# Kernel tuning notes

Measured on AMD Instinct MI355X. Metric: run time of the kernel, lower is better.

## Reference

```python
import jax, jax.numpy as jnp
import numpy as np

N_NODES = 50000
NEG_SLOPE = 0.2


def gat_conv(x, W, att_src, att_dst, b, src, dst, n):
    # x: [N, F_in], W: [F_in, H*C], att_*: [H, C], b: [H*C]
    H, C = att_src.shape
    h = (x @ W).reshape(n, H, C)                       # [N, H, C]
    a_s = (h * att_src).sum(-1)                        # [N, H]
    a_d = (h * att_dst).sum(-1)                        # [N, H]
    e = jax.nn.leaky_relu(a_s[src] + a_d[dst], NEG_SLOPE)  # [E, H]
    # segment softmax over destination node (every node has a self-loop)
    m = jax.ops.segment_max(e, dst, num_segments=n)    # [N, H]
    ex = jnp.exp(e - m[dst])
    denom = jax.ops.segment_sum(ex, dst, num_segments=n)
    alpha = ex / denom[dst]                            # [E, H]
    out = jax.ops.segment_sum(alpha[:, :, None] * h[src], dst, num_segments=n)
    return out.reshape(n, H * C) + b


def setup_inputs() -> dict:
    key = jax.random.key(0)
    ks = jax.random.split(key, 10)
    n, e = N_NODES, 1600000
    x = jax.random.normal(ks[0], (n, 128), dtype=jnp.float32)
    edge_index = jax.random.randint(ks[1], (2, e), 0, n, dtype=jnp.int64)
    s = 0.1
    return {
        "x": x,
        "edge_index": edge_index,
        "W1": jax.random.normal(ks[2], (128, 128), dtype=jnp.float32) * s,
        "att_src1": jax.random.normal(ks[3], (4, 32), dtype=jnp.float32) * s,
        "att_dst1": jax.random.normal(ks[4], (4, 32), dtype=jnp.float32) * s,
        "b1": jnp.zeros((128,), dtype=jnp.float32),
        "W2": jax.random.normal(ks[5], (128, 128), dtype=jnp.float32) * s,
        "att_src2": jax.random.normal(ks[6], (4, 32), dtype=jnp.float32) * s,
        "att_dst2": jax.random.normal(ks[7], (4, 32), dtype=jnp.float32) * s,
        "b2": jnp.zeros((128,), dtype=jnp.float32),
    }


def reference(x, edge_index, W1, att_src1, att_dst1, b1, W2, att_src2, att_dst2, b2):
    n = x.shape[0]
    loops = jnp.arange(n, dtype=edge_index.dtype)
    src = jnp.concatenate([edge_index[0], loops])  # add self-loops (PyG default)
    dst = jnp.concatenate([edge_index[1], loops])
    h = gat_conv(x, W1, att_src1, att_dst1, b1, src, dst, n)
    h = jax.nn.relu(h)
    h = gat_conv(h, W2, att_src2, att_dst2, b2, src, dst, n)
    return (h, h)
```

## Files before the change

kernel.cpp:

```cpp
#include <hip/hip_runtime.h>
#include <hip/hip_bf16.h>


#define FDIM 128
#define NHEAD 4
#define NB 512

typedef __attribute__((ext_vector_type(16))) float f32x16;
typedef __attribute__((ext_vector_type(8)))  short s16x8;

__device__ inline unsigned short f2bf(float f) {
    union { float f; unsigned u; } v; v.f = f;
    unsigned r = v.u + 0x7fff + ((v.u >> 16) & 1);
    return (unsigned short)(r >> 16);
}
__device__ inline float2 bf2f(unsigned v) {
    union { unsigned u; float f; } a, b;
    a.u = v << 16;
    b.u = v & 0xffff0000u;
    return make_float2(a.f, b.f);
}

__global__ __launch_bounds__(256) void prep_w(const float* __restrict__ W,
                                              short* __restrict__ Bhi,
                                              short* __restrict__ Blo) {
    const int t = threadIdx.x;
    for (int i = 0; i < 64; i++) {
        int e = i * 256 + t;
        int k = e >> 7, n = e & 127;
        float f = W[e];
        unsigned u = __float_as_uint(f);
        unsigned short hi = (unsigned short)(u >> 16);
        float rem = f - __uint_as_float(u & 0xffff0000u);
        unsigned short lo = (unsigned short)(__float_as_uint(rem) >> 16);
        int idx = n * 128 + ((((k >> 3) ^ (n & 15))) << 3) + (k & 7);
        Bhi[idx] = (short)hi;
        Blo[idx] = (short)lo;
    }
}

__global__ __launch_bounds__(256) void gemm_mfma(const float* __restrict__ A,
                                                 const short* __restrict__ Bghi,
                                                 const short* __restrict__ Bglo,
                                                 unsigned short* __restrict__ H,
                                                 const float* __restrict__ att_s,
                                                 const float* __restrict__ att_d,
                                                 float* __restrict__ a_s,
                                                 float* __restrict__ a_d, int M) {
    __shared__ short Bsm[2][16384];
    __shared__ float attsm[256];
    const int t = threadIdx.x;
    const int bm = blockIdx.x * 64;

    if (t < 128) attsm[t] = att_s[t];
    else         attsm[t] = att_d[t - 128];

    {
        const uint4* ghi = (const uint4*)Bghi;
        const uint4* glo = (const uint4*)Bglo;
        uint4* shi = (uint4*)&Bsm[0][0];
        uint4* slo = (uint4*)&Bsm[1][0];
        #pragma unroll
        for (int i = 0; i < 8; i++) {
            shi[t + i * 256] = ghi[t + i * 256];
            slo[t + i * 256] = glo[t + i * 256];
        }
    }

    const int lane = t & 63;
    const int w = t >> 6;
    const int wr = w >> 1, wc = w & 1;
    const int m  = lane & 31, h2 = lane >> 5;
    const int grow = bm + wr * 32 + m;

    s16x8 ahi[8], alo[8];
    {
        const bool ok = grow < M;
        const float* ap = A + (size_t)grow * 128 + 8 * h2;
        #pragma unroll
        for (int c = 0; c < 8; c++) {
            float ff[8];
            if (ok) {
                float4 f0 = *(const float4*)(ap + c * 16);
                float4 f1 = *(const float4*)(ap + c * 16 + 4);
                ff[0]=f0.x; ff[1]=f0.y; ff[2]=f0.z; ff[3]=f0.w;
                ff[4]=f1.x; ff[5]=f1.y; ff[6]=f1.z; ff[7]=f1.w;
            } else {
                #pragma unroll
                for (int j = 0; j < 8; j++) ff[j] = 0.f;
            }
            #pragma unroll
            for (int j = 0; j < 8; j++) {
                unsigned u = __float_as_uint(ff[j]);
                float rem = ff[j] - __uint_as_float(u & 0xffff0000u);
                ahi[c][j] = (short)(u >> 16);
                alo[c][j] = (short)(__float_as_uint(rem) >> 16);
            }
        }
    }
    __syncthreads();

    f32x16 acc[2];
    #pragma unroll
    for (int i = 0; i < 16; i++) { acc[0][i] = 0.f; acc[1][i] = 0.f; }

    #pragma unroll
    for (int ni = 0; ni < 2; ni++) {
        const int n = ni * 64 + wc * 32 + m;
        const int nbase = n * 128;
        #pragma unroll
        for (int c = 0; c < 8; c++) {
            int chunk8 = 2 * c + h2;
            int koff = ((chunk8 ^ (n & 15)) << 3);
            s16x8 bhi = *(const s16x8*)&Bsm[0][nbase + koff];
            s16x8 blo = *(const s16x8*)&Bsm[1][nbase + koff];
            acc[ni] = __builtin_amdgcn_mfma_f32_32x32x16_bf16(ahi[c], bhi, acc[ni], 0, 0, 0);
            acc[ni] = __builtin_amdgcn_mfma_f32_32x32x16_bf16(alo[c], bhi, acc[ni], 0, 0, 0);
            acc[ni] = __builtin_amdgcn_mfma_f32_32x32x16_bf16(ahi[c], blo, acc[ni], 0, 0, 0);
        }
    }

    __syncthreads();
    unsigned short* htile = (unsigned short*)&Bsm[0][0];
    #pragma unroll
    for (int ni = 0; ni < 2; ni++) {
        const int colg = ni * 64 + wc * 32 + m;
        #pragma unroll
        for (int r = 0; r < 16; r++) {
            int row = wr * 32 + (r & 3) + 8 * (r >> 2) + 4 * h2;
            htile[row * 128 + colg] = (short)f2bf(acc[ni][r]);
        }
    }
    __syncthreads();

    {
        const int r = t >> 2, q = t & 3;
        const int growr = bm + r;
        if (growr < M) {
            uint4 v0 = *(uint4*)&htile[r * 128 + q * 32];
            uint4 v1 = *(uint4*)&htile[r * 128 + q * 32 + 8];
            uint4 v2 = *(uint4*)&htile[r * 128 + q * 32 + 16];
            uint4 v3 = *(uint4*)&htile[r * 128 + q * 32 + 24];
            uint4* hg = (uint4*)(H + (size_t)growr * 128);
            hg[q * 4 + 0] = v0; hg[q * 4 + 1] = v1;
            hg[q * 4 + 2] = v2; hg[q * 4 + 3] = v3;
            unsigned uu[16] = {v0.x, v0.y, v0.z, v0.w, v1.x, v1.y, v1.z, v1.w,
                               v2.x, v2.y, v2.z, v2.w, v3.x, v3.y, v3.z, v3.w};
            float ps = 0.f, pd = 0.f;
            #pragma unroll
            for (int i = 0; i < 16; i++) {
                float2 f = bf2f(uu[i]);
                ps += f.x * attsm[q * 32 + 2 * i]       + f.y * attsm[q * 32 + 2 * i + 1];
                pd += f.x * attsm[128 + q * 32 + 2 * i] + f.y * attsm[128 + q * 32 + 2 * i + 1];
            }
            a_s[growr * NHEAD + q] = ps;
            a_d[growr * NHEAD + q] = pd;
        }
    }
}

__global__ __launch_bounds__(256) void bucket_hist(const int* __restrict__ dst, int E,
                                                   unsigned long long magic,
                                                   int* __restrict__ bcnt) {
    __shared__ int sh[NB];
    const int t = threadIdx.x;
    for (int i = t; i < NB; i += 256) sh[i] = 0;
    __syncthreads();
    for (int i = blockIdx.x * blockDim.x + t; i < E; i += gridDim.x * blockDim.x) {
        int b = (int)(((unsigned long long)(unsigned)dst[i] * magic) >> 40);
        atomicAdd(&sh[b], 1);
    }
    __syncthreads();
    for (int i = t; i < NB; i += 256)
        if (sh[i]) atomicAdd(&bcnt[i], sh[i]);
}

__global__ __launch_bounds__(256) void bucket_scan(const int* __restrict__ bcnt,
                                                   int* __restrict__ bbase,
                                                   int* __restrict__ bcursor,
                                                   int* __restrict__ row_ptr,
                                                   int N, int E) {
    __shared__ int wsum[4];
    const int t = threadIdx.x, lane = t & 63, wid = t >> 6;
    int v0 = bcnt[2 * t], v1 = bcnt[2 * t + 1];
    int s = v0 + v1, incl = s;
    #pragma unroll
    for (int o = 1; o < 64; o <<= 1) {
        int u = __shfl_up(incl, o, 64);
        if (lane >= o) incl += u;
    }
    if (lane == 63) wsum[wid] = incl;
    __syncthreads();
    if (t == 0) {
        int a = 0;
        #pragma unroll
        for (int i = 0; i < 4; i++) { int x = wsum[i]; wsum[i] = a; a += x; }
    }
    __syncthreads();
    int excl = wsum[wid] + incl - s;
    bbase[2 * t] = excl;          bcursor[2 * t] = excl;
    bbase[2 * t + 1] = excl + v0; bcursor[2 * t + 1] = excl + v0;
    if (t == 0) { bbase[NB] = E; row_ptr[N] = E; }
}

__global__ __launch_bounds__(256) void partition(const int* __restrict__ src,
                                                 const int* __restrict__ dst, int E,
                                                 unsigned long long magic,
                                                 int* __restrict__ bcursor,
                                                 int2* __restrict__ ebuf) {
    __shared__ int shc[NB];
    __shared__ int shb[NB];
    __shared__ int shcur[NB];
    const int t = threadIdx.x;
    for (int i = t; i < NB; i += 256) shc[i] = 0;
    __syncthreads();
    const int e0 = blockIdx.x * 4096;
    int myb[16], mys[16], myd[16];
    #pragma unroll
    for (int u = 0; u < 16; u++) {
        int i = e0 + u * 256 + t;
        if (i < E) {
            mys[u] = src[i];
            myd[u] = dst[i];
            int b = (int)(((unsigned long long)(unsigned)myd[u] * magic) >> 40);
            myb[u] = b;
            atomicAdd(&shc[b], 1);
        } else myb[u] = -1;
    }
    __syncthreads();
    for (int i = t; i < NB; i += 256) {
        int c = shc[i];
        shcur[i] = 0;
        if (c) shb[i] = atomicAdd(&bcursor[i], c);
    }
    __syncthreads();
    #pragma unroll
    for (int u = 0; u < 16; u++) {
        if (myb[u] >= 0) {
            int o = atomicAdd(&shcur[myb[u]], 1);
            ebuf[shb[myb[u]] + o] = make_int2(mys[u], myd[u]);
        }
    }
}

__global__ __launch_bounds__(256) void build_bucket(const int2* __restrict__ ebuf,
                                                    const int* __restrict__ bbase,
                                                    int npb, int N,
                                                    int* __restrict__ row_ptr,
                                                    int* __restrict__ col) {
    __shared__ int degl[256];
    __shared__ int curl[256];
    const int b = blockIdx.x;
    const int t = threadIdx.x, lane = t & 63, wid = t >> 6;
    const int base = bbase[b];
    const int cnt = bbase[b + 1] - base;
    const int node0 = b * npb;
    for (int i = t; i < npb; i += 256) degl[i] = 0;
    __syncthreads();
    for (int i = t; i < cnt; i += 256) {
        int d = ebuf[base + i].y;
        atomicAdd(&degl[d - node0], 1);
    }
    __syncthreads();
    if (wid == 0) {
        int run = 0;
        for (int c = 0; c * 64 < npb; c++) {
            int idx = c * 64 + lane;
            int v = (idx < npb) ? degl[idx] : 0;
            int incl = v;
            #pragma unroll
            for (int o = 1; o < 64; o <<= 1) {
                int u = __shfl_up(incl, o, 64);
                if (lane >= o) incl += u;
            }
            int excl = incl - v + run;
            if (idx < npb) {
                curl[idx] = excl;
                int node = node0 + idx;
                if (node < N) row_ptr[node] = base + excl;
            }
            run += __shfl(incl, 63, 64);
        }
    }
    __syncthreads();
    for (int i = t; i < cnt; i += 256) {
        int2 ed = ebuf[base + i];
        int p = atomicAdd(&curl[ed.y - node0], 1);
        col[base + p] = ed.x;
    }
}

__global__ __launch_bounds__(64) void aggregate(const unsigned short* __restrict__ h,
                                                const float* __restrict__ a_s,
                                                const float* __restrict__ a_d,
                                                const int* __restrict__ row_ptr,
                                                const int* __restrict__ col,
                                                const float* __restrict__ bias,
                                                float* __restrict__ out,
                                                float* __restrict__ out2,
                                                int n, int do_relu) {
    const int nid = blockIdx.x;
    const int c = threadIdx.x;
    const int hd = c >> 4;
    const float ad = a_d[nid * NHEAD + hd];
    const unsigned* __restrict__ h2 = (const unsigned*)h;

    float e = a_s[nid * NHEAD + hd] + ad;
    e = (e > 0.f) ? e : 0.2f * e;
    float den = __expf(e);
    float2 hv = bf2f(h2[(size_t)nid * 64 + c]);
    float num0 = den * hv.x, num1 = den * hv.y;

    const int beg = row_ptr[nid], end = row_ptr[nid + 1];
    int j = beg;
    for (; j + 8 <= end; j += 8) {
        int s[8];
        #pragma unroll
        for (int u = 0; u < 8; u++) s[u] = col[j + u];
        unsigned v[8]; float el[8];
        #pragma unroll
        for (int u = 0; u < 8; u++) v[u] = h2[(size_t)s[u] * 64 + c];
        #pragma unroll
        for (int u = 0; u < 8; u++) el[u] = a_s[s[u] * NHEAD + hd];
        #pragma unroll
        for (int u = 0; u < 8; u++) {
            float e2 = el[u] + ad;
            e2 = (e2 > 0.f) ? e2 : 0.2f * e2;
            float wgt = __expf(e2);
            den += wgt;
            float2 f = bf2f(v[u]);
            num0 += wgt * f.x;
            num1 += wgt * f.y;
        }
    }
    for (; j < end; j++) {
        int s = col[j];
        float e2 = a_s[s * NHEAD + hd] + ad;
        e2 = (e2 > 0.f) ? e2 : 0.2f * e2;
        float wgt = __expf(e2);
        den += wgt;
        float2 f = bf2f(h2[(size_t)s * 64 + c]);
        num0 += wgt * f.x;
        num1 += wgt * f.y;
    }
    float2 bv = ((const float2*)bias)[c];
    float rd = 1.0f / den;
    float o0 = num0 * rd + bv.x;
    float o1 = num1 * rd + bv.y;
    if (do_relu) { o0 = fmaxf(o0, 0.f); o1 = fmaxf(o1, 0.f); }
    ((float2*)out)[(size_t)nid * 64 + c] = make_float2(o0, o1);
    if (out2) ((float2*)out2)[(size_t)nid * 64 + c] = make_float2(o0, o1);
}

extern "C" void kernel_launch(void* const* d_in, const int* in_sizes, int n_in,
                              void* d_out, int out_size, void* d_ws, size_t ws_size,
                              hipStream_t stream) {
    const float* x        = (const float*)d_in[0];
    const int*   edge     = (const int*)d_in[1];
    const float* W1       = (const float*)d_in[2];
    const float* att_s1   = (const float*)d_in[3];
    const float* att_d1   = (const float*)d_in[4];
    const float* b1       = (const float*)d_in[5];
    const float* W2       = (const float*)d_in[6];
    const float* att_s2   = (const float*)d_in[7];
    const float* att_d2   = (const float*)d_in[8];
    const float* b2       = (const float*)d_in[9];
    float* out = (float*)d_out;

    const int N = in_sizes[0] / FDIM;
    const int E = in_sizes[1] / 2;
    const int* src = edge;
    const int* dst = edge + E;

    const int npb = (N + NB - 1) / NB;
    const unsigned long long magic = ((1ull << 40) / (unsigned long long)npb) + 1;

    char* w = (char*)d_ws;
    size_t off = 0;
    auto alloc = [&](size_t bytes) { void* p = w + off; off = (off + bytes + 255) & ~(size_t)255; return p; };
    int*   row_ptr = (int*)alloc((size_t)(N + 1) * 4);
    int*   col     = (int*)alloc((size_t)E * 4);
    int*   bcnt    = (int*)alloc((size_t)NB * 4);
    int*   bbase   = (int*)alloc((size_t)(NB + 1) * 4);
    int*   bcursor = (int*)alloc((size_t)NB * 4);
    unsigned short* h1 = (unsigned short*)alloc((size_t)N * FDIM * 2);
    float* hx      = (float*)alloc((size_t)N * FDIM * 4);
    float* as1     = (float*)alloc((size_t)N * NHEAD * 4);
    float* ad1     = (float*)alloc((size_t)N * NHEAD * 4);
    float* as2     = (float*)alloc((size_t)N * NHEAD * 4);
    float* ad2     = (float*)alloc((size_t)N * NHEAD * 4);
    short* Bg1hi   = (short*)alloc((size_t)128 * 128 * 2);
    short* Bg1lo   = (short*)alloc((size_t)128 * 128 * 2);
    short* Bg2hi   = (short*)alloc((size_t)128 * 128 * 2);
    short* Bg2lo   = (short*)alloc((size_t)128 * 128 * 2);
    int2*  ebuf    = (int2*)hx;
    (void)ws_size;

    prep_w<<<1, 256, 0, stream>>>(W1, Bg1hi, Bg1lo);
    prep_w<<<1, 256, 0, stream>>>(W2, Bg2hi, Bg2lo);

    hipMemsetAsync(bcnt, 0, (size_t)NB * 4, stream);
    bucket_hist<<<1024, 256, 0, stream>>>(dst, E, magic, bcnt);
    bucket_scan<<<1, 256, 0, stream>>>(bcnt, bbase, bcursor, row_ptr, N, E);
    partition<<<(E + 4095) / 4096, 256, 0, stream>>>(src, dst, E, magic, bcursor, ebuf);
    build_bucket<<<NB, 256, 0, stream>>>(ebuf, bbase, npb, N, row_ptr, col);

    const int gblocks = (N + 63) / 64;

    gemm_mfma<<<gblocks, 256, 0, stream>>>(x, Bg1hi, Bg1lo, h1, att_s1, att_d1, as1, ad1, N);
    aggregate<<<N, 64, 0, stream>>>(h1, as1, ad1, row_ptr, col, b1, hx, nullptr, N, 1);

    gemm_mfma<<<gblocks, 256, 0, stream>>>(hx, Bg2hi, Bg2lo, h1, att_s2, att_d2, as2, ad2, N);
    aggregate<<<N, 64, 0, stream>>>(h1, as2, ad2, row_ptr, col, b2,
                                    out, out + (size_t)N * FDIM, N, 0);
}
```

Baseline: 348.6 us.

## Precompute per-edge attention weights in separate kernel; fuse weight prep with histogram

```diff
diff --git a/kernel.cpp b/kernel.cpp
--- a/kernel.cpp
+++ b/kernel.cpp
@@ -20,23 +20,48 @@
     b.u = v & 0xffff0000u;
     return make_float2(a.f, b.f);
 }
-
-__global__ __launch_bounds__(256) void prep_w(const float* __restrict__ W,
-                                              short* __restrict__ Bhi,
-                                              short* __restrict__ Blo) {
+__device__ inline void splitbf(float f, short* hi, short* lo) {
+    unsigned u = __float_as_uint(f);
+    float rem = f - __uint_as_float(u & 0xffff0000u);
+    *hi = (short)(u >> 16);
+    *lo = (short)(__float_as_uint(rem) >> 16);
+}
+
+__global__ __launch_bounds__(256) void prep_hist(const float* __restrict__ W1,
+                                                 short* __restrict__ B1hi,
+                                                 short* __restrict__ B1lo,
+                                                 const float* __restrict__ W2,
+                                                 short* __restrict__ B2hi,
+                                                 short* __restrict__ B2lo,
+                                                 const int* __restrict__ dst, int E,
+                                                 unsigned long long magic,
+                                                 int* __restrict__ bcnt) {
+    __shared__ int sh[NB];
     const int t = threadIdx.x;
-    for (int i = 0; i < 64; i++) {
-        int e = i * 256 + t;
+    const int b = blockIdx.x;
+    if (b < 128) {
+        const float* W = (b < 64) ? W1 : W2;
+        short* Bhi = (b < 64) ? B1hi : B2hi;
+        short* Blo = (b < 64) ? B1lo : B2lo;
+        int e = (b & 63) * 256 + t;
         int k = e >> 7, n = e & 127;
-        float f = W[e];
-        unsigned u = __float_as_uint(f);
-        unsigned short hi = (unsigned short)(u >> 16);
-        float rem = f - __uint_as_float(u & 0xffff0000u);
-        unsigned short lo = (unsigned short)(__float_as_uint(rem) >> 16);
-        int idx = n * 128 + ((((k >> 3) ^ (n & 15))) << 3) + (k & 7);
-        Bhi[idx] = (short)hi;
-        Blo[idx] = (short)lo;
-    }
+        short hi, lo;
+        splitbf(W[e], &hi, &lo);
+        int idx = n * 128 + (((k >> 3) ^ (n & 15)) << 3) + (k & 7);
+        Bhi[idx] = hi;
+        Blo[idx] = lo;
+        return;
+    }
+    for (int i = t; i < NB; i += 256) sh[i] = 0;
+    __syncthreads();
+    const int stride = (gridDim.x - 128) * 256;
+    for (int i = (b - 128) * 256 + t; i < E; i += stride) {
+        int bk = (int)(((unsigned long long)(unsigned)dst[i] * magic) >> 40);
+        atomicAdd(&sh[bk], 1);
+    }
+    __syncthreads();
+    for (int i = t; i < NB; i += 256)
+        if (sh[i]) atomicAdd(&bcnt[i], sh[i]);
 }
 
 __global__ __launch_bounds__(256) void gemm_mfma(const float* __restrict__ A,
@@ -91,10 +116,10 @@
             }
             #pragma unroll
             for (int j = 0; j < 8; j++) {
-                unsigned u = __float_as_uint(ff[j]);
-                float rem = ff[j] - __uint_as_float(u & 0xffff0000u);
-                ahi[c][j] = (short)(u >> 16);
-                alo[c][j] = (short)(__float_as_uint(rem) >> 16);
+                short hi, lo;
+                splitbf(ff[j], &hi, &lo);
+                ahi[c][j] = hi;
+                alo[c][j] = lo;
             }
         }
     }
@@ -159,22 +184,6 @@
     }
 }
 
-__global__ __launch_bounds__(256) void bucket_hist(const int* __restrict__ dst, int E,
-                                                   unsigned long long magic,
-                                                   int* __restrict__ bcnt) {
-    __shared__ int sh[NB];
-    const int t = threadIdx.x;
-    for (int i = t; i < NB; i += 256) sh[i] = 0;
-    __syncthreads();
-    for (int i = blockIdx.x * blockDim.x + t; i < E; i += gridDim.x * blockDim.x) {
-        int b = (int)(((unsigned long long)(unsigned)dst[i] * magic) >> 40);
-        atomicAdd(&sh[b], 1);
-    }
-    __syncthreads();
-    for (int i = t; i < NB; i += 256)
-        if (sh[i]) atomicAdd(&bcnt[i], sh[i]);
-}
-
 __global__ __launch_bounds__(256) void bucket_scan(const int* __restrict__ bcnt,
                                                    int* __restrict__ bbase,
                                                    int* __restrict__ bcursor,
@@ -247,7 +256,8 @@
                                                     const int* __restrict__ bbase,
                                                     int npb, int N,
                                                     int* __restrict__ row_ptr,
-                                                    int* __restrict__ col) {
+                                                    int* __restrict__ col,
+                                                    int* __restrict__ edst) {
     __shared__ int degl[256];
     __shared__ int curl[256];
     const int b = blockIdx.x;
@@ -287,7 +297,23 @@
         int2 ed = ebuf[base + i];
         int p = atomicAdd(&curl[ed.y - node0], 1);
         col[base + p] = ed.x;
-    }
+        edst[base + p] = ed.y;
+    }
+}
+
+__global__ __launch_bounds__(256) void edge_w(const int* __restrict__ col,
+                                              const int* __restrict__ edst,
+                                              const float4* __restrict__ as4,
+                                              const float4* __restrict__ ad4,
+                                              int E, float4* __restrict__ w4) {
+    int i = blockIdx.x * 256 + threadIdx.x;
+    if (i >= E) return;
+    float4 a = as4[col[i]];
+    float4 b = ad4[edst[i]];
+    float ex = a.x + b.x, ey = a.y + b.y, ez = a.z + b.z, ew = a.w + b.w;
+    ex = fmaxf(ex, 0.2f * ex); ey = fmaxf(ey, 0.2f * ey);
+    ez = fmaxf(ez, 0.2f * ez); ew = fmaxf(ew, 0.2f * ew);
+    w4[i] = make_float4(__expf(ex), __expf(ey), __expf(ez), __expf(ew));
 }
 
 __global__ __launch_bounds__(64) void aggregate(const unsigned short* __restrict__ h,
@@ -295,6 +321,7 @@
                                                 const float* __restrict__ a_d,
                                                 const int* __restrict__ row_ptr,
                                                 const int* __restrict__ col,
+                                                const float* __restrict__ wbuf,
                                                 const float* __restrict__ bias,
                                                 float* __restrict__ out,
                                                 float* __restrict__ out2,
@@ -302,11 +329,10 @@
     const int nid = blockIdx.x;
     const int c = threadIdx.x;
     const int hd = c >> 4;
-    const float ad = a_d[nid * NHEAD + hd];
     const unsigned* __restrict__ h2 = (const unsigned*)h;
 
-    float e = a_s[nid * NHEAD + hd] + ad;
-    e = (e > 0.f) ? e : 0.2f * e;
+    float e = a_s[nid * NHEAD + hd] + a_d[nid * NHEAD + hd];
+    e = fmaxf(e, 0.2f * e);
     float den = __expf(e);
     float2 hv = bf2f(h2[(size_t)nid * 64 + c]);
     float num0 = den * hv.x, num1 = den * hv.y;
@@ -317,27 +343,22 @@
         int s[8];
         #pragma unroll
         for (int u = 0; u < 8; u++) s[u] = col[j + u];
-        unsigned v[8]; float el[8];
+        unsigned v[8]; float wv[8];
         #pragma unroll
         for (int u = 0; u < 8; u++) v[u] = h2[(size_t)s[u] * 64 + c];
         #pragma unroll
-        for (int u = 0; u < 8; u++) el[u] = a_s[s[u] * NHEAD + hd];
+        for (int u = 0; u < 8; u++) wv[u] = wbuf[(size_t)(j + u) * 4 + hd];
         #pragma unroll
         for (int u = 0; u < 8; u++) {
-            float e2 = el[u] + ad;
-            e2 = (e2 > 0.f) ? e2 : 0.2f * e2;
-            float wgt = __expf(e2);
-            den += wgt;
+            den += wv[u];
             float2 f = bf2f(v[u]);
-            num0 += wgt * f.x;
-            num1 += wgt * f.y;
+            num0 += wv[u] * f.x;
+            num1 += wv[u] * f.y;
         }
     }
     for (; j < end; j++) {
         int s = col[j];
-        float e2 = a_s[s * NHEAD + hd] + ad;
-        e2 = (e2 > 0.f) ? e2 : 0.2f * e2;
-        float wgt = __expf(e2);
+        float wgt = wbuf[(size_t)j * 4 + hd];
         den += wgt;
         float2 f = bf2f(h2[(size_t)s * 64 + c]);
         num0 += wgt * f.x;
@@ -380,6 +401,8 @@
     auto alloc = [&](size_t bytes) { void* p = w + off; off = (off + bytes + 255) & ~(size_t)255; return p; };
     int*   row_ptr = (int*)alloc((size_t)(N + 1) * 4);
     int*   col     = (int*)alloc((size_t)E * 4);
+    int*   edst    = (int*)alloc((size_t)E * 4);
+    float* wbuf    = (float*)alloc((size_t)E * 4 * 4);
     int*   bcnt    = (int*)alloc((size_t)NB * 4);
     int*   bbase   = (int*)alloc((size_t)(NB + 1) * 4);
     int*   bcursor = (int*)alloc((size_t)NB * 4);
@@ -396,21 +419,25 @@
     int2*  ebuf    = (int2*)hx;
     (void)ws_size;
 
-    prep_w<<<1, 256, 0, stream>>>(W1, Bg1hi, Bg1lo);
-    prep_w<<<1, 256, 0, stream>>>(W2, Bg2hi, Bg2lo);
-
     hipMemsetAsync(bcnt, 0, (size_t)NB * 4, stream);
-    bucket_hist<<<1024, 256, 0, stream>>>(dst, E, magic, bcnt);
+    prep_hist<<<128 + 1024, 256, 0, stream>>>(W1, Bg1hi, Bg1lo, W2, Bg2hi, Bg2lo,
+                                              dst, E, magic, bcnt);
     bucket_scan<<<1, 256, 0, stream>>>(bcnt, bbase, bcursor, row_ptr, N, E);
     partition<<<(E + 4095) / 4096, 256, 0, stream>>>(src, dst, E, magic, bcursor, ebuf);
-    build_bucket<<<NB, 256, 0, stream>>>(ebuf, bbase, npb, N, row_ptr, col);
+    build_bucket<<<NB, 256, 0, stream>>>(ebuf, bbase, npb, N, row_ptr, col, edst);
 
     const int gblocks = (N + 63) / 64;
+    const int eb = (E + 255) / 256;
 
     gemm_mfma<<<gblocks, 256, 0, stream>>>(x, Bg1hi, Bg1lo, h1, att_s1, att_d1, as1, ad1, N);
-    aggregate<<<N, 64, 0, stream>>>(h1, as1, ad1, row_ptr, col, b1, hx, nullptr, N, 1);
+    edge_w<<<eb, 256, 0, stream>>>(col, edst, (const float4*)as1, (const float4*)ad1,
+                                   E, (float4*)wbuf);
+    aggregate<<<N, 64, 0, stream>>>(h1, as1, ad1, row_ptr, col, wbuf, b1,
+                                    hx, nullptr, N, 1);
 
     gemm_mfma<<<gblocks, 256, 0, stream>>>(hx, Bg2hi, Bg2lo, h1, att_s2, att_d2, as2, ad2, N);
-    aggregate<<<N, 64, 0, stream>>>(h1, as2, ad2, row_ptr, col, b2,
+    edge_w<<<eb, 256, 0, stream>>>(col, edst, (const float4*)as2, (const float4*)ad2,
+                                   E, (float4*)wbuf);
+    aggregate<<<N, 64, 0, stream>>>(h1, as2, ad2, row_ptr, col, wbuf, b2,
                                     out, out + (size_t)N * FDIM, N, 0);
 }
```

Result: faster. 338.1 us (-3.0%).
